# Kernel optimization log

Hardware: AMD Instinct MI355X
Metric: run time of the kernel (lower is better)

The kernel has to match this reference:

```python
import jax, jax.numpy as jnp
import numpy as np

ALPHA = 1.0  # Student-t degrees of freedom (module default)


def setup_inputs() -> dict:
    key = jax.random.key(0)
    k1, k2 = jax.random.split(key)
    N, D, K = 65536, 512, 256
    x = jax.random.normal(k1, (N, D), dtype=jnp.float32)
    clusters = jax.random.normal(k2, (K, D), dtype=jnp.float32)
    return {"x": x, "clusters": clusters}


def reference(x, clusters):
    # Squared Euclidean distance via norm expansion + GEMM (same math as
    # sum((x[:,None,:] - clusters[None,:,:])**2, axis=2); original then takes
    # sqrt and immediately re-squares, so we use sqdist directly).
    x_sq = jnp.sum(x * x, axis=1, keepdims=True)            # [N,1]
    c_sq = jnp.sum(clusters * clusters, axis=1)             # [K]
    sqdist = x_sq + c_sq[None, :] - 2.0 * (x @ clusters.T)  # [N,K]
    sqdist = jnp.maximum(sqdist, 0.0)
    # Student's t kernel: q_ij = (1 + d^2/alpha)^(-(alpha+1)/2)
    q = (1.0 + sqdist / ALPHA) ** (-(ALPHA + 1.0) / 2.0)
    # Row-normalize to soft assignments
    return q / jnp.sum(q, axis=1, keepdims=True)
```

## Files before the change

### kernel.cpp

```cpp
#include <hip/hip_runtime.h>
#include <hip/hip_bf16.h>
#include <stdint.h>

typedef unsigned short u16;
typedef __attribute__((ext_vector_type(8))) short short8_t;
typedef __attribute__((ext_vector_type(4))) float f32x4;

#define D_DIM 512
#define K_CL  256
#define BM    128

__device__ __forceinline__ u16 f2bf(float f) {
  union { float f; uint32_t u; } v; v.f = f;
  uint32_t r = v.u + 0x7fffu + ((v.u >> 16) & 1u);
  return (u16)(r >> 16);
}

__global__ void prep_kernel(const float* __restrict__ clusters,
                            u16* __restrict__ cb, float* __restrict__ csq) {
  int k = blockIdx.x;
  int t = threadIdx.x;
  float4 f = ((const float4*)(clusters + (size_t)k * D_DIM))[t];
  ushort4 u;
  u.x = f2bf(f.x); u.y = f2bf(f.y); u.z = f2bf(f.z); u.w = f2bf(f.w);
  ((ushort4*)(cb + (size_t)k * D_DIM))[t] = u;
  float s = f.x*f.x + f.y*f.y + f.z*f.z + f.w*f.w;
  #pragma unroll
  for (int m = 1; m < 64; m <<= 1) s += __shfl_xor(s, m, 64);
  __shared__ float part[2];
  if ((t & 63) == 0) part[t >> 6] = s;
  __syncthreads();
  if (t == 0) csq[k] = part[0] + part[1];
}

__global__ __launch_bounds__(512)
void cluster_kernel(const float* __restrict__ x,
                    const u16* __restrict__ cb,
                    const float* __restrict__ csq,
                    float* __restrict__ out) {
  __shared__ u16  lA[BM * 32];
  __shared__ u16  lB[K_CL * 32];
  __shared__ float xsq_lds[BM];
  __shared__ float csq_lds[K_CL];
  __shared__ float rowsum[4 * BM];

  const int tid   = threadIdx.x;
  const int lane  = tid & 63;
  const int w     = tid >> 6;
  const int quad  = lane >> 4;
  const int l16   = lane & 15;
  const int wave_m = w >> 2;
  const int wave_n = w & 3;
  const int row0  = blockIdx.x * BM;

  if (tid < K_CL) csq_lds[tid] = csq[tid];

  const int ar = tid >> 2;
  const int ac = (tid & 3) * 8;
  const float* xg = x + (size_t)(row0 + ar) * D_DIM + ac;
  short8_t* aw = (short8_t*)&lA[ar * 32 + ac];

  const int aro = (wave_m * 64 + l16) * 32 + quad * 8;
  const int bro = (wave_n * 64 + l16) * 32 + quad * 8;

  f32x4 acc[4][4];
  #pragma unroll
  for (int i = 0; i < 4; ++i)
    #pragma unroll
    for (int j = 0; j < 4; ++j)
      acc[i][j] = (f32x4){0.f, 0.f, 0.f, 0.f};

  float sq = 0.f;
  const int boff0 = tid * 16;

  for (int kk = 0; kk < D_DIM; kk += 32) {
    if (kk) __syncthreads();
    float4 f0 = *(const float4*)(xg + kk);
    float4 f1 = *(const float4*)(xg + kk + 4);
    sq += f0.x*f0.x + f0.y*f0.y + f0.z*f0.z + f0.w*f0.w
        + f1.x*f1.x + f1.y*f1.y + f1.z*f1.z + f1.w*f1.w;
    union { u16 u[8]; short8_t v; } pk;
    pk.u[0]=f2bf(f0.x); pk.u[1]=f2bf(f0.y); pk.u[2]=f2bf(f0.z); pk.u[3]=f2bf(f0.w);
    pk.u[4]=f2bf(f1.x); pk.u[5]=f2bf(f1.y); pk.u[6]=f2bf(f1.z); pk.u[7]=f2bf(f1.w);
    *aw = pk.v;
    #pragma unroll
    for (int i = 0; i < 2; ++i) {
      int off = boff0 + i * 8192;
      int n = off >> 6;
      int inrow = off & 63;
      const u16* src = cb + (size_t)n * D_DIM + kk + (inrow >> 1);
      __builtin_amdgcn_global_load_lds(
          (const __attribute__((address_space(1))) void*)src,
          (__attribute__((address_space(3))) void*)((char*)lB + off),
          16, 0, 0);
    }
    __syncthreads();
    short8_t aF[4], bF[4];
    #pragma unroll
    for (int mi = 0; mi < 4; ++mi)
      aF[mi] = *(const short8_t*)&lA[aro + mi * 16 * 32];
    #pragma unroll
    for (int ni = 0; ni < 4; ++ni)
      bF[ni] = *(const short8_t*)&lB[bro + ni * 16 * 32];
    #pragma unroll
    for (int mi = 0; mi < 4; ++mi)
      #pragma unroll
      for (int ni = 0; ni < 4; ++ni)
        acc[mi][ni] = __builtin_amdgcn_mfma_f32_16x16x32_bf16(
            aF[mi], bF[ni], acc[mi][ni], 0, 0, 0);
  }

  sq += __shfl_xor(sq, 1, 64);
  sq += __shfl_xor(sq, 2, 64);
  if ((tid & 3) == 0) xsq_lds[ar] = sq;
  __syncthreads();

  #pragma unroll
  for (int mi = 0; mi < 4; ++mi) {
    #pragma unroll
    for (int v = 0; v < 4; ++v) {
      int row = wave_m * 64 + mi * 16 + quad * 4 + v;
      float xs = xsq_lds[row];
      float s = 0.f;
      #pragma unroll
      for (int ni = 0; ni < 4; ++ni) {
        int col = wave_n * 64 + ni * 16 + l16;
        float d = xs + csq_lds[col] - 2.0f * acc[mi][ni][v];
        d = fmaxf(d, 0.f);
        float q = 1.0f / (1.0f + d);
        acc[mi][ni][v] = q;
        s += q;
      }
      s += __shfl_xor(s, 1, 64);
      s += __shfl_xor(s, 2, 64);
      s += __shfl_xor(s, 4, 64);
      s += __shfl_xor(s, 8, 64);
      if (l16 == 0) rowsum[wave_n * BM + row] = s;
    }
  }
  __syncthreads();

  #pragma unroll
  for (int mi = 0; mi < 4; ++mi) {
    #pragma unroll
    for (int v = 0; v < 4; ++v) {
      int row = wave_m * 64 + mi * 16 + quad * 4 + v;
      float tot = rowsum[row] + rowsum[BM + row] + rowsum[2*BM + row] + rowsum[3*BM + row];
      float inv = 1.0f / tot;
      float* orow = out + (size_t)(row0 + row) * K_CL;
      #pragma unroll
      for (int ni = 0; ni < 4; ++ni) {
        int col = wave_n * 64 + ni * 16 + l16;
        orow[col] = acc[mi][ni][v] * inv;
      }
    }
  }
}

extern "C" void kernel_launch(void* const* d_in, const int* in_sizes, int n_in,
                              void* d_out, int out_size, void* d_ws, size_t ws_size,
                              hipStream_t stream) {
  const float* x        = (const float*)d_in[0];
  const float* clusters = (const float*)d_in[1];
  float* out = (float*)d_out;
  const int N = in_sizes[0] / D_DIM;

  u16*   cb  = (u16*)d_ws;
  float* csq = (float*)((char*)d_ws + (size_t)K_CL * D_DIM * sizeof(u16));

  prep_kernel<<<K_CL, 128, 0, stream>>>(clusters, cb, csq);
  cluster_kernel<<<N / BM, 512, 0, stream>>>(x, cb, csq, out);
}
```

Measured before the change: 217.9 us.

## Double-buffer LDS tiles with XOR swizzle and halve block rows

Restructures the GEMM main loop so the A and B tiles live in double-buffered LDS. The next k-slice of the bf16 cluster tile is prefetched via global_load_lds, and the next x values are held in registers while MFMAs run on the current buffer, which drops one barrier per iteration. LDS addresses get an XOR swizzle to cut bank conflicts on the fragment reads. Blocks shrink to 64 rows and 256 threads, giving more blocks and higher occupancy, at the cost of re-reading the cluster tile from L2 twice as often per row.

```diff
diff --git a/kernel.cpp b/kernel.cpp
--- a/kernel.cpp
+++ b/kernel.cpp
@@ -8,7 +8,8 @@
 
 #define D_DIM 512
 #define K_CL  256
-#define BM    128
+#define BM    64
+#define NITER 16
 
 __device__ __forceinline__ u16 f2bf(float f) {
   union { float f; uint32_t u; } v; v.f = f;
@@ -33,35 +34,39 @@
   if (t == 0) csq[k] = part[0] + part[1];
 }
 
-__global__ __launch_bounds__(512)
+__global__ __launch_bounds__(256)
 void cluster_kernel(const float* __restrict__ x,
                     const u16* __restrict__ cb,
                     const float* __restrict__ csq,
                     float* __restrict__ out) {
-  __shared__ u16  lA[BM * 32];
-  __shared__ u16  lB[K_CL * 32];
-  __shared__ float xsq_lds[BM];
-  __shared__ float csq_lds[K_CL];
-  __shared__ float rowsum[4 * BM];
-
-  const int tid   = threadIdx.x;
-  const int lane  = tid & 63;
-  const int w     = tid >> 6;
-  const int quad  = lane >> 4;
-  const int l16   = lane & 15;
-  const int wave_m = w >> 2;
-  const int wave_n = w & 3;
-  const int row0  = blockIdx.x * BM;
-
-  if (tid < K_CL) csq_lds[tid] = csq[tid];
-
-  const int ar = tid >> 2;
-  const int ac = (tid & 3) * 8;
-  const float* xg = x + (size_t)(row0 + ar) * D_DIM + ac;
-  short8_t* aw = (short8_t*)&lA[ar * 32 + ac];
-
-  const int aro = (wave_m * 64 + l16) * 32 + quad * 8;
-  const int bro = (wave_n * 64 + l16) * 32 + quad * 8;
+  __shared__ __align__(16) char smem[8192 + 32768];
+  float* xsq    = (float*)smem;
+  float* rowsum = (float*)(smem + 256);
+
+  const int tid  = threadIdx.x;
+  const int lane = tid & 63;
+  const int w    = tid >> 6;
+  const int quad = lane >> 4;
+  const int l16  = lane & 15;
+  const int row0 = blockIdx.x * BM;
+  const int sl    = (l16 ^ (l16 >> 2)) & 3;
+  const int slotq = quad ^ sl;
+
+  const int ar  = tid >> 2;
+  const int jga = tid & 3;
+  const int sa  = (ar ^ (ar >> 2)) & 3;
+  const float* xg = x + (size_t)(row0 + ar) * D_DIM + jga * 8;
+  const int awoff = ar * 64 + ((jga ^ sa) * 16);
+
+  const u16* bsrc[4];
+  #pragma unroll
+  for (int i = 0; i < 4; ++i) {
+    int L = i * 256 + tid;
+    int c  = L >> 2;
+    int jp = L & 3;
+    int jg = jp ^ ((c ^ (c >> 2)) & 3);
+    bsrc[i] = cb + (size_t)c * D_DIM + jg * 8;
+  }
 
   f32x4 acc[4][4];
   #pragma unroll
@@ -71,61 +76,93 @@
       acc[i][j] = (f32x4){0.f, 0.f, 0.f, 0.f};
 
   float sq = 0.f;
-  const int boff0 = tid * 16;
-
-  for (int kk = 0; kk < D_DIM; kk += 32) {
-    if (kk) __syncthreads();
-    float4 f0 = *(const float4*)(xg + kk);
-    float4 f1 = *(const float4*)(xg + kk + 4);
+  float4 xr[2][2];
+
+  #pragma unroll
+  for (int i = 0; i < 4; ++i)
+    __builtin_amdgcn_global_load_lds(
+        (const __attribute__((address_space(1))) void*)bsrc[i],
+        (__attribute__((address_space(3))) void*)(smem + 8192 + (i * 256 + tid) * 16),
+        16, 0, 0);
+  {
+    float4 f0 = *(const float4*)(xg + 0);
+    float4 f1 = *(const float4*)(xg + 4);
     sq += f0.x*f0.x + f0.y*f0.y + f0.z*f0.z + f0.w*f0.w
         + f1.x*f1.x + f1.y*f1.y + f1.z*f1.z + f1.w*f1.w;
     union { u16 u[8]; short8_t v; } pk;
     pk.u[0]=f2bf(f0.x); pk.u[1]=f2bf(f0.y); pk.u[2]=f2bf(f0.z); pk.u[3]=f2bf(f0.w);
     pk.u[4]=f2bf(f1.x); pk.u[5]=f2bf(f1.y); pk.u[6]=f2bf(f1.z); pk.u[7]=f2bf(f1.w);
-    *aw = pk.v;
-    #pragma unroll
-    for (int i = 0; i < 2; ++i) {
-      int off = boff0 + i * 8192;
-      int n = off >> 6;
-      int inrow = off & 63;
-      const u16* src = cb + (size_t)n * D_DIM + kk + (inrow >> 1);
-      __builtin_amdgcn_global_load_lds(
-          (const __attribute__((address_space(1))) void*)src,
-          (__attribute__((address_space(3))) void*)((char*)lB + off),
-          16, 0, 0);
-    }
+    *(short8_t*)(smem + awoff) = pk.v;
+  }
+  xr[1][0] = *(const float4*)(xg + 32);
+  xr[1][1] = *(const float4*)(xg + 36);
+
+  #pragma unroll
+  for (int kk16 = 0; kk16 < NITER; ++kk16) {
+    const int b  = kk16 & 1;
+    const int kk = kk16 * 32;
     __syncthreads();
+
+    if (kk16 < NITER - 1) {
+      #pragma unroll
+      for (int i = 0; i < 4; ++i)
+        __builtin_amdgcn_global_load_lds(
+            (const __attribute__((address_space(1))) void*)(bsrc[i] + kk + 32),
+            (__attribute__((address_space(3))) void*)
+                (smem + 8192 + (b ^ 1) * 16384 + (i * 256 + tid) * 16),
+            16, 0, 0);
+    }
+    if (kk16 < NITER - 2) {
+      xr[b][0] = *(const float4*)(xg + kk + 64);
+      xr[b][1] = *(const float4*)(xg + kk + 68);
+    }
+
     short8_t aF[4], bF[4];
     #pragma unroll
     for (int mi = 0; mi < 4; ++mi)
-      aF[mi] = *(const short8_t*)&lA[aro + mi * 16 * 32];
+      aF[mi] = *(const short8_t*)(smem + b * 4096 + mi * 1024 + l16 * 64 + slotq * 16);
     #pragma unroll
     for (int ni = 0; ni < 4; ++ni)
-      bF[ni] = *(const short8_t*)&lB[bro + ni * 16 * 32];
+      bF[ni] = *(const short8_t*)(smem + 8192 + b * 16384 + w * 4096 + ni * 1024
+                                  + l16 * 64 + slotq * 16);
     #pragma unroll
     for (int mi = 0; mi < 4; ++mi)
       #pragma unroll
       for (int ni = 0; ni < 4; ++ni)
         acc[mi][ni] = __builtin_amdgcn_mfma_f32_16x16x32_bf16(
             aF[mi], bF[ni], acc[mi][ni], 0, 0, 0);
+
+    if (kk16 < NITER - 1) {
+      float4 f0 = xr[b ^ 1][0];
+      float4 f1 = xr[b ^ 1][1];
+      sq += f0.x*f0.x + f0.y*f0.y + f0.z*f0.z + f0.w*f0.w
+          + f1.x*f1.x + f1.y*f1.y + f1.z*f1.z + f1.w*f1.w;
+      union { u16 u[8]; short8_t v; } pk;
+      pk.u[0]=f2bf(f0.x); pk.u[1]=f2bf(f0.y); pk.u[2]=f2bf(f0.z); pk.u[3]=f2bf(f0.w);
+      pk.u[4]=f2bf(f1.x); pk.u[5]=f2bf(f1.y); pk.u[6]=f2bf(f1.z); pk.u[7]=f2bf(f1.w);
+      *(short8_t*)(smem + (b ^ 1) * 4096 + awoff) = pk.v;
+    }
   }
 
   sq += __shfl_xor(sq, 1, 64);
   sq += __shfl_xor(sq, 2, 64);
-  if ((tid & 3) == 0) xsq_lds[ar] = sq;
+  if ((tid & 3) == 0) xsq[ar] = sq;
   __syncthreads();
 
+  float cs[4];
+  #pragma unroll
+  for (int ni = 0; ni < 4; ++ni) cs[ni] = csq[w * 64 + ni * 16 + l16];
+
   #pragma unroll
   for (int mi = 0; mi < 4; ++mi) {
     #pragma unroll
     for (int v = 0; v < 4; ++v) {
-      int row = wave_m * 64 + mi * 16 + quad * 4 + v;
-      float xs = xsq_lds[row];
+      int row = mi * 16 + quad * 4 + v;
+      float xs = xsq[row];
       float s = 0.f;
       #pragma unroll
       for (int ni = 0; ni < 4; ++ni) {
-        int col = wave_n * 64 + ni * 16 + l16;
-        float d = xs + csq_lds[col] - 2.0f * acc[mi][ni][v];
+        float d = xs + cs[ni] - 2.0f * acc[mi][ni][v];
         d = fmaxf(d, 0.f);
         float q = 1.0f / (1.0f + d);
         acc[mi][ni][v] = q;
@@ -135,7 +172,7 @@
       s += __shfl_xor(s, 2, 64);
       s += __shfl_xor(s, 4, 64);
       s += __shfl_xor(s, 8, 64);
-      if (l16 == 0) rowsum[wave_n * BM + row] = s;
+      if (l16 == 0) rowsum[w * 64 + row] = s;
     }
   }
   __syncthreads();
@@ -144,15 +181,13 @@
   for (int mi = 0; mi < 4; ++mi) {
     #pragma unroll
     for (int v = 0; v < 4; ++v) {
-      int row = wave_m * 64 + mi * 16 + quad * 4 + v;
-      float tot = rowsum[row] + rowsum[BM + row] + rowsum[2*BM + row] + rowsum[3*BM + row];
+      int row = mi * 16 + quad * 4 + v;
+      float tot = rowsum[row] + rowsum[64 + row] + rowsum[128 + row] + rowsum[192 + row];
       float inv = 1.0f / tot;
       float* orow = out + (size_t)(row0 + row) * K_CL;
       #pragma unroll
-      for (int ni = 0; ni < 4; ++ni) {
-        int col = wave_n * 64 + ni * 16 + l16;
-        orow[col] = acc[mi][ni][v] * inv;
-      }
+      for (int ni = 0; ni < 4; ++ni)
+        orow[w * 64 + ni * 16 + l16] = acc[mi][ni][v] * inv;
     }
   }
 }
@@ -169,5 +204,5 @@
   float* csq = (float*)((char*)d_ws + (size_t)K_CL * D_DIM * sizeof(u16));
 
   prep_kernel<<<K_CL, 128, 0, stream>>>(clusters, cb, csq);
-  cluster_kernel<<<N / BM, 512, 0, stream>>>(x, cb, csq, out);
-}
+  cluster_kernel<<<N / BM, 256, 0, stream>>>(x, cb, csq, out);
+}
```

Result: slower. 247.8 us (+13.7%).

## Load MFMA operands directly from global into registers, drop LDS staging

Applied to the files above, without the earlier changes.

The GEMM no longer stages through LDS. Each wave loads its A and B fragments straight from global memory into registers, with a register double-buffered prefetch, and the per-step block barriers are gone. Each block now covers 64 rows with 4 waves, and each wave computes 32 rows by 128 clusters. The x row norms are reduced with shuffles instead of LDS, and output uses nontemporal stores. The aim is to remove barrier and LDS traffic overhead. In exchange, B fragments are re-fetched per wave from L2, and register pressure rises.

```diff
diff --git a/kernel.cpp b/kernel.cpp
--- a/kernel.cpp
+++ b/kernel.cpp
@@ -8,7 +8,7 @@
 
 #define D_DIM 512
 #define K_CL  256
-#define BM    128
+#define STEPS 16
 
 __device__ __forceinline__ u16 f2bf(float f) {
   union { float f; uint32_t u; } v; v.f = f;
@@ -33,99 +33,103 @@
   if (t == 0) csq[k] = part[0] + part[1];
 }
 
-__global__ __launch_bounds__(512)
+__global__ __launch_bounds__(256)
 void cluster_kernel(const float* __restrict__ x,
                     const u16* __restrict__ cb,
                     const float* __restrict__ csq,
                     float* __restrict__ out) {
-  __shared__ u16  lA[BM * 32];
-  __shared__ u16  lB[K_CL * 32];
-  __shared__ float xsq_lds[BM];
-  __shared__ float csq_lds[K_CL];
-  __shared__ float rowsum[4 * BM];
+  __shared__ float rowsum[2][2][32];
 
-  const int tid   = threadIdx.x;
-  const int lane  = tid & 63;
-  const int w     = tid >> 6;
-  const int quad  = lane >> 4;
-  const int l16   = lane & 15;
-  const int wave_m = w >> 2;
-  const int wave_n = w & 3;
-  const int row0  = blockIdx.x * BM;
+  const int tid    = threadIdx.x;
+  const int lane   = tid & 63;
+  const int w      = tid >> 6;
+  const int stripe = w >> 1;
+  const int half   = w & 1;
+  const int quad   = lane >> 4;
+  const int l16    = lane & 15;
+  const int row0   = blockIdx.x * 64 + stripe * 32;
 
-  if (tid < K_CL) csq_lds[tid] = csq[tid];
+  const float* xg0 = x + (size_t)(row0 + l16) * D_DIM + quad * 8;
+  const float* xg1 = xg0 + 16 * D_DIM;
 
-  const int ar = tid >> 2;
-  const int ac = (tid & 3) * 8;
-  const float* xg = x + (size_t)(row0 + ar) * D_DIM + ac;
-  short8_t* aw = (short8_t*)&lA[ar * 32 + ac];
+  const u16* bg[8];
+  #pragma unroll
+  for (int ni = 0; ni < 8; ++ni)
+    bg[ni] = cb + (size_t)(half * 128 + ni * 16 + l16) * D_DIM + quad * 8;
 
-  const int aro = (wave_m * 64 + l16) * 32 + quad * 8;
-  const int bro = (wave_n * 64 + l16) * 32 + quad * 8;
+  f32x4 acc[2][8];
+  #pragma unroll
+  for (int mi = 0; mi < 2; ++mi)
+    #pragma unroll
+    for (int ni = 0; ni < 8; ++ni)
+      acc[mi][ni] = (f32x4){0.f, 0.f, 0.f, 0.f};
 
-  f32x4 acc[4][4];
+  float sq0 = 0.f, sq1 = 0.f;
+
+  short8_t Bp[2][8];
+  float4   Ap[2][4];
   #pragma unroll
-  for (int i = 0; i < 4; ++i)
+  for (int ni = 0; ni < 8; ++ni) Bp[0][ni] = *(const short8_t*)(bg[ni]);
+  Ap[0][0] = *(const float4*)(xg0);
+  Ap[0][1] = *(const float4*)(xg0 + 4);
+  Ap[0][2] = *(const float4*)(xg1);
+  Ap[0][3] = *(const float4*)(xg1 + 4);
+
+  #pragma unroll
+  for (int k = 0; k < STEPS; ++k) {
+    const int cur = k & 1, nxt = cur ^ 1;
+    if (k < STEPS - 1) {
+      #pragma unroll
+      for (int ni = 0; ni < 8; ++ni)
+        Bp[nxt][ni] = *(const short8_t*)(bg[ni] + (k + 1) * 32);
+      Ap[nxt][0] = *(const float4*)(xg0 + (k + 1) * 32);
+      Ap[nxt][1] = *(const float4*)(xg0 + (k + 1) * 32 + 4);
+      Ap[nxt][2] = *(const float4*)(xg1 + (k + 1) * 32);
+      Ap[nxt][3] = *(const float4*)(xg1 + (k + 1) * 32 + 4);
+    }
+    short8_t aF0, aF1;
+    {
+      float4 f0 = Ap[cur][0], f1 = Ap[cur][1];
+      sq0 += f0.x*f0.x + f0.y*f0.y + f0.z*f0.z + f0.w*f0.w
+           + f1.x*f1.x + f1.y*f1.y + f1.z*f1.z + f1.w*f1.w;
+      union { u16 u[8]; short8_t v; } pk;
+      pk.u[0]=f2bf(f0.x); pk.u[1]=f2bf(f0.y); pk.u[2]=f2bf(f0.z); pk.u[3]=f2bf(f0.w);
+      pk.u[4]=f2bf(f1.x); pk.u[5]=f2bf(f1.y); pk.u[6]=f2bf(f1.z); pk.u[7]=f2bf(f1.w);
+      aF0 = pk.v;
+    }
+    {
+      float4 f0 = Ap[cur][2], f1 = Ap[cur][3];
+      sq1 += f0.x*f0.x + f0.y*f0.y + f0.z*f0.z + f0.w*f0.w
+           + f1.x*f1.x + f1.y*f1.y + f1.z*f1.z + f1.w*f1.w;
+      union { u16 u[8]; short8_t v; } pk;
+      pk.u[0]=f2bf(f0.x); pk.u[1]=f2bf(f0.y); pk.u[2]=f2bf(f0.z); pk.u[3]=f2bf(f0.w);
+      pk.u[4]=f2bf(f1.x); pk.u[5]=f2bf(f1.y); pk.u[6]=f2bf(f1.z); pk.u[7]=f2bf(f1.w);
+      aF1 = pk.v;
+    }
     #pragma unroll
-    for (int j = 0; j < 4; ++j)
-      acc[i][j] = (f32x4){0.f, 0.f, 0.f, 0.f};
-
-  float sq = 0.f;
-  const int boff0 = tid * 16;
-
-  for (int kk = 0; kk < D_DIM; kk += 32) {
-    if (kk) __syncthreads();
-    float4 f0 = *(const float4*)(xg + kk);
-    float4 f1 = *(const float4*)(xg + kk + 4);
-    sq += f0.x*f0.x + f0.y*f0.y + f0.z*f0.z + f0.w*f0.w
-        + f1.x*f1.x + f1.y*f1.y + f1.z*f1.z + f1.w*f1.w;
-    union { u16 u[8]; short8_t v; } pk;
-    pk.u[0]=f2bf(f0.x); pk.u[1]=f2bf(f0.y); pk.u[2]=f2bf(f0.z); pk.u[3]=f2bf(f0.w);
-    pk.u[4]=f2bf(f1.x); pk.u[5]=f2bf(f1.y); pk.u[6]=f2bf(f1.z); pk.u[7]=f2bf(f1.w);
-    *aw = pk.v;
-    #pragma unroll
-    for (int i = 0; i < 2; ++i) {
-      int off = boff0 + i * 8192;
-      int n = off >> 6;
-      int inrow = off & 63;
-      const u16* src = cb + (size_t)n * D_DIM + kk + (inrow >> 1);
-      __builtin_amdgcn_global_load_lds(
-          (const __attribute__((address_space(1))) void*)src,
-          (__attribute__((address_space(3))) void*)((char*)lB + off),
-          16, 0, 0);
+    for (int ni = 0; ni < 8; ++ni) {
+      acc[0][ni] = __builtin_amdgcn_mfma_f32_16x16x32_bf16(aF0, Bp[cur][ni], acc[0][ni], 0, 0, 0);
+      acc[1][ni] = __builtin_amdgcn_mfma_f32_16x16x32_bf16(aF1, Bp[cur][ni], acc[1][ni], 0, 0, 0);
     }
-    __syncthreads();
-    short8_t aF[4], bF[4];
-    #pragma unroll
-    for (int mi = 0; mi < 4; ++mi)
-      aF[mi] = *(const short8_t*)&lA[aro + mi * 16 * 32];
-    #pragma unroll
-    for (int ni = 0; ni < 4; ++ni)
-      bF[ni] = *(const short8_t*)&lB[bro + ni * 16 * 32];
-    #pragma unroll
-    for (int mi = 0; mi < 4; ++mi)
-      #pragma unroll
-      for (int ni = 0; ni < 4; ++ni)
-        acc[mi][ni] = __builtin_amdgcn_mfma_f32_16x16x32_bf16(
-            aF[mi], bF[ni], acc[mi][ni], 0, 0, 0);
   }
 
-  sq += __shfl_xor(sq, 1, 64);
-  sq += __shfl_xor(sq, 2, 64);
-  if ((tid & 3) == 0) xsq_lds[ar] = sq;
-  __syncthreads();
+  sq0 += __shfl_xor(sq0, 16, 64); sq0 += __shfl_xor(sq0, 32, 64);
+  sq1 += __shfl_xor(sq1, 16, 64); sq1 += __shfl_xor(sq1, 32, 64);
+
+  float cs[8];
+  #pragma unroll
+  for (int ni = 0; ni < 8; ++ni) cs[ni] = csq[half * 128 + ni * 16 + l16];
 
   #pragma unroll
-  for (int mi = 0; mi < 4; ++mi) {
+  for (int mi = 0; mi < 2; ++mi) {
     #pragma unroll
     for (int v = 0; v < 4; ++v) {
-      int row = wave_m * 64 + mi * 16 + quad * 4 + v;
-      float xs = xsq_lds[row];
+      const int r = quad * 4 + v;
+      const float xs = __shfl(mi == 0 ? sq0 : sq1, r, 64);
       float s = 0.f;
       #pragma unroll
-      for (int ni = 0; ni < 4; ++ni) {
-        int col = wave_n * 64 + ni * 16 + l16;
-        float d = xs + csq_lds[col] - 2.0f * acc[mi][ni][v];
+      for (int ni = 0; ni < 8; ++ni) {
+        float d = xs + cs[ni] - 2.0f * acc[mi][ni][v];
         d = fmaxf(d, 0.f);
         float q = 1.0f / (1.0f + d);
         acc[mi][ni][v] = q;
@@ -135,24 +139,21 @@
       s += __shfl_xor(s, 2, 64);
       s += __shfl_xor(s, 4, 64);
       s += __shfl_xor(s, 8, 64);
-      if (l16 == 0) rowsum[wave_n * BM + row] = s;
+      if (l16 == 0) rowsum[stripe][half][mi * 16 + r] = s;
     }
   }
   __syncthreads();
 
   #pragma unroll
-  for (int mi = 0; mi < 4; ++mi) {
+  for (int mi = 0; mi < 2; ++mi) {
     #pragma unroll
     for (int v = 0; v < 4; ++v) {
-      int row = wave_m * 64 + mi * 16 + quad * 4 + v;
-      float tot = rowsum[row] + rowsum[BM + row] + rowsum[2*BM + row] + rowsum[3*BM + row];
-      float inv = 1.0f / tot;
-      float* orow = out + (size_t)(row0 + row) * K_CL;
+      const int r = mi * 16 + quad * 4 + v;
+      const float inv = 1.0f / (rowsum[stripe][0][r] + rowsum[stripe][1][r]);
+      float* orow = out + (size_t)(row0 + r) * K_CL + half * 128;
       #pragma unroll
-      for (int ni = 0; ni < 4; ++ni) {
-        int col = wave_n * 64 + ni * 16 + l16;
-        orow[col] = acc[mi][ni][v] * inv;
-      }
+      for (int ni = 0; ni < 8; ++ni)
+        __builtin_nontemporal_store(acc[mi][ni][v] * inv, orow + ni * 16 + l16);
     }
   }
 }
@@ -169,5 +170,5 @@
   float* csq = (float*)((char*)d_ws + (size_t)K_CL * D_DIM * sizeof(u16));
 
   prep_kernel<<<K_CL, 128, 0, stream>>>(clusters, cb, csq);
-  cluster_kernel<<<N / BM, 512, 0, stream>>>(x, cb, csq, out);
+  cluster_kernel<<<N / 64, 256, 0, stream>>>(x, cb, csq, out);
 }
```

New measurement: 321.0 us. 47.3% more time.

## Shrink row tile to 64 with 256-thread blocks, prefetch x, nontemporal stores

Applied to the files above, without the earlier changes.

Halves the row tile to 64 rows and runs 256-thread blocks, each wave owning a 64-column slice of all 64 rows. Launch bounds ask for 4 blocks per CU to raise occupancy. The next x chunk is loaded into registers one iteration ahead, so global latency overlaps the MFMA work. Output writes use nontemporal stores to cut cache pollution. In exchange, the cluster matrix is reloaded from L2 twice as often per row, since there are twice as many blocks.

```diff
diff --git a/kernel.cpp b/kernel.cpp
--- a/kernel.cpp
+++ b/kernel.cpp
@@ -8,7 +8,8 @@
 
 #define D_DIM 512
 #define K_CL  256
-#define BM    128
+#define BM    64
+#define NITER 16
 
 __device__ __forceinline__ u16 f2bf(float f) {
   union { float f; uint32_t u; } v; v.f = f;
@@ -33,7 +34,7 @@
   if (t == 0) csq[k] = part[0] + part[1];
 }
 
-__global__ __launch_bounds__(512)
+__global__ __launch_bounds__(256, 4)
 void cluster_kernel(const float* __restrict__ x,
                     const u16* __restrict__ cb,
                     const float* __restrict__ csq,
@@ -44,24 +45,21 @@
   __shared__ float csq_lds[K_CL];
   __shared__ float rowsum[4 * BM];
 
-  const int tid   = threadIdx.x;
-  const int lane  = tid & 63;
-  const int w     = tid >> 6;
-  const int quad  = lane >> 4;
-  const int l16   = lane & 15;
-  const int wave_m = w >> 2;
-  const int wave_n = w & 3;
-  const int row0  = blockIdx.x * BM;
+  const int tid  = threadIdx.x;
+  const int lane = tid & 63;
+  const int w    = tid >> 6;
+  const int quad = lane >> 4;
+  const int l16  = lane & 15;
+  const int row0 = blockIdx.x * BM;
 
-  if (tid < K_CL) csq_lds[tid] = csq[tid];
+  csq_lds[tid] = csq[tid];
 
-  const int ar = tid >> 2;
-  const int ac = (tid & 3) * 8;
-  const float* xg = x + (size_t)(row0 + ar) * D_DIM + ac;
-  short8_t* aw = (short8_t*)&lA[ar * 32 + ac];
+  const int ar  = tid >> 2;
+  const int jga = tid & 3;
+  const float* xg = x + (size_t)(row0 + ar) * D_DIM + jga * 8;
+  short8_t* aw = (short8_t*)&lA[ar * 32 + jga * 8];
 
-  const int aro = (wave_m * 64 + l16) * 32 + quad * 8;
-  const int bro = (wave_n * 64 + l16) * 32 + quad * 8;
+  const u16* bsrc0 = cb + (size_t)ar * D_DIM + jga * 8;
 
   f32x4 acc[4][4];
   #pragma unroll
@@ -71,43 +69,51 @@
       acc[i][j] = (f32x4){0.f, 0.f, 0.f, 0.f};
 
   float sq = 0.f;
-  const int boff0 = tid * 16;
 
-  for (int kk = 0; kk < D_DIM; kk += 32) {
-    if (kk) __syncthreads();
-    float4 f0 = *(const float4*)(xg + kk);
-    float4 f1 = *(const float4*)(xg + kk + 4);
-    sq += f0.x*f0.x + f0.y*f0.y + f0.z*f0.z + f0.w*f0.w
-        + f1.x*f1.x + f1.y*f1.y + f1.z*f1.z + f1.w*f1.w;
-    union { u16 u[8]; short8_t v; } pk;
-    pk.u[0]=f2bf(f0.x); pk.u[1]=f2bf(f0.y); pk.u[2]=f2bf(f0.z); pk.u[3]=f2bf(f0.w);
-    pk.u[4]=f2bf(f1.x); pk.u[5]=f2bf(f1.y); pk.u[6]=f2bf(f1.z); pk.u[7]=f2bf(f1.w);
-    *aw = pk.v;
+  float4 f0 = *(const float4*)(xg);
+  float4 f1 = *(const float4*)(xg + 4);
+
+  #pragma unroll 1
+  for (int k = 0; k < NITER; ++k) {
+    const int kk = k * 32;
+
     #pragma unroll
-    for (int i = 0; i < 2; ++i) {
-      int off = boff0 + i * 8192;
-      int n = off >> 6;
-      int inrow = off & 63;
-      const u16* src = cb + (size_t)n * D_DIM + kk + (inrow >> 1);
+    for (int i = 0; i < 4; ++i)
       __builtin_amdgcn_global_load_lds(
-          (const __attribute__((address_space(1))) void*)src,
-          (__attribute__((address_space(3))) void*)((char*)lB + off),
+          (const __attribute__((address_space(1))) void*)(bsrc0 + i * (64 * D_DIM) + kk),
+          (__attribute__((address_space(3))) void*)((char*)lB + (i * 256 + tid) * 16),
           16, 0, 0);
+
+    {
+      sq += f0.x*f0.x + f0.y*f0.y + f0.z*f0.z + f0.w*f0.w
+          + f1.x*f1.x + f1.y*f1.y + f1.z*f1.z + f1.w*f1.w;
+      union { u16 u[8]; short8_t v; } pk;
+      pk.u[0]=f2bf(f0.x); pk.u[1]=f2bf(f0.y); pk.u[2]=f2bf(f0.z); pk.u[3]=f2bf(f0.w);
+      pk.u[4]=f2bf(f1.x); pk.u[5]=f2bf(f1.y); pk.u[6]=f2bf(f1.z); pk.u[7]=f2bf(f1.w);
+      *aw = pk.v;
     }
+
+    if (k < NITER - 1) {
+      f0 = *(const float4*)(xg + kk + 32);
+      f1 = *(const float4*)(xg + kk + 36);
+    }
+
     __syncthreads();
-    short8_t aF[4], bF[4];
+
+    short8_t aF[4];
     #pragma unroll
     for (int mi = 0; mi < 4; ++mi)
-      aF[mi] = *(const short8_t*)&lA[aro + mi * 16 * 32];
+      aF[mi] = *(const short8_t*)&lA[(mi * 16 + l16) * 32 + quad * 8];
     #pragma unroll
-    for (int ni = 0; ni < 4; ++ni)
-      bF[ni] = *(const short8_t*)&lB[bro + ni * 16 * 32];
-    #pragma unroll
-    for (int mi = 0; mi < 4; ++mi)
+    for (int ni = 0; ni < 4; ++ni) {
+      short8_t bF = *(const short8_t*)&lB[(w * 64 + ni * 16 + l16) * 32 + quad * 8];
       #pragma unroll
-      for (int ni = 0; ni < 4; ++ni)
+      for (int mi = 0; mi < 4; ++mi)
         acc[mi][ni] = __builtin_amdgcn_mfma_f32_16x16x32_bf16(
-            aF[mi], bF[ni], acc[mi][ni], 0, 0, 0);
+            aF[mi], bF, acc[mi][ni], 0, 0, 0);
+    }
+
+    if (k < NITER - 1) __syncthreads();
   }
 
   sq += __shfl_xor(sq, 1, 64);
@@ -119,13 +125,12 @@
   for (int mi = 0; mi < 4; ++mi) {
     #pragma unroll
     for (int v = 0; v < 4; ++v) {
-      int row = wave_m * 64 + mi * 16 + quad * 4 + v;
+      int row = mi * 16 + quad * 4 + v;
       float xs = xsq_lds[row];
       float s = 0.f;
       #pragma unroll
       for (int ni = 0; ni < 4; ++ni) {
-        int col = wave_n * 64 + ni * 16 + l16;
-        float d = xs + csq_lds[col] - 2.0f * acc[mi][ni][v];
+        float d = xs + csq_lds[w * 64 + ni * 16 + l16] - 2.0f * acc[mi][ni][v];
         d = fmaxf(d, 0.f);
         float q = 1.0f / (1.0f + d);
         acc[mi][ni][v] = q;
@@ -135,7 +140,7 @@
       s += __shfl_xor(s, 2, 64);
       s += __shfl_xor(s, 4, 64);
       s += __shfl_xor(s, 8, 64);
-      if (l16 == 0) rowsum[wave_n * BM + row] = s;
+      if (l16 == 0) rowsum[w * 64 + row] = s;
     }
   }
   __syncthreads();
@@ -144,15 +149,14 @@
   for (int mi = 0; mi < 4; ++mi) {
     #pragma unroll
     for (int v = 0; v < 4; ++v) {
-      int row = wave_m * 64 + mi * 16 + quad * 4 + v;
-      float tot = rowsum[row] + rowsum[BM + row] + rowsum[2*BM + row] + rowsum[3*BM + row];
+      int row = mi * 16 + quad * 4 + v;
+      float tot = rowsum[row] + rowsum[64 + row] + rowsum[128 + row] + rowsum[192 + row];
       float inv = 1.0f / tot;
       float* orow = out + (size_t)(row0 + row) * K_CL;
       #pragma unroll
-      for (int ni = 0; ni < 4; ++ni) {
-        int col = wave_n * 64 + ni * 16 + l16;
-        orow[col] = acc[mi][ni][v] * inv;
-      }
+      for (int ni = 0; ni < 4; ++ni)
+        __builtin_nontemporal_store(acc[mi][ni][v] * inv,
+                                    orow + w * 64 + ni * 16 + l16);
     }
   }
 }
@@ -169,5 +173,5 @@
   float* csq = (float*)((char*)d_ws + (size_t)K_CL * D_DIM * sizeof(u16));
 
   prep_kernel<<<K_CL, 128, 0, stream>>>(clusters, cb, csq);
-  cluster_kernel<<<N / BM, 512, 0, stream>>>(x, cb, csq, out);
+  cluster_kernel<<<N / BM, 256, 0, stream>>>(x, cb, csq, out);
 }
```

Result: slower. 232.3 us (+6.6%).
